# Performance work log

Measured on AMD Instinct MI355X. Metric: run time of the kernel, lower is better.

## Reference

```python
import jax, jax.numpy as jnp
import numpy as np

B, T, IN_DIM = 32, 512, 16
F_DIM, N_AGG, N_HEADS = 128, 32, 4


def _ln(x, g, b, eps=1e-5):
    m = jnp.mean(x, axis=-1, keepdims=True)
    v = jnp.var(x, axis=-1, keepdims=True)
    return (x - m) * jax.lax.rsqrt(v + eps) * g + b


def _masked_sab(X, mask, wq, bq, wk, bk, wv, bv, wo, bo, g0, be0, g1, be1):
    # Set-Transformer style SAB = MAB(X, X) with key-side masking.
    Bn, Tn, _ = X.shape
    Dh = F_DIM // N_HEADS
    Q = X @ wq + bq
    K = X @ wk + bk
    V = X @ wv + bv
    Qh = Q.reshape(Bn, Tn, N_HEADS, Dh)
    Kh = K.reshape(Bn, Tn, N_HEADS, Dh)
    Vh = V.reshape(Bn, Tn, N_HEADS, Dh)
    scores = jnp.einsum('bqhd,bkhd->bhqk', Qh, Kh) / np.float32(np.sqrt(Dh))
    scores = jnp.where(mask[:, None, None, :] > 0, scores, jnp.float32(-1e9))
    A = jax.nn.softmax(scores, axis=-1)
    O = Q + jnp.einsum('bhqk,bkhd->bqhd', A, Vh).reshape(Bn, Tn, F_DIM)
    O = _ln(O, g0, be0)
    O = O + jax.nn.relu(O @ wo + bo)
    return _ln(O, g1, be1)


def setup_inputs():
    key = jax.random.key(0)
    ks = list(jax.random.split(key, 16))

    def g(k, shape):
        return jax.random.uniform(k, shape, jnp.float32, -1.0, 1.0) / np.float32(np.sqrt(shape[0]))

    inp = {
        'X': jax.random.normal(ks[0], (B, T, IN_DIM), dtype=jnp.float32),
        'mask': jax.random.bernoulli(ks[1], 0.8, (B, T)).astype(jnp.float32),
    }
    i = 2
    for suf, din in (('0', IN_DIM), ('1', F_DIM)):
        kk = jax.random.split(ks[i], 4); i += 1
        inp['wq' + suf] = g(kk[0], (din, F_DIM)); inp['bq' + suf] = jnp.zeros((F_DIM,), jnp.float32)
        inp['wk' + suf] = g(kk[1], (din, F_DIM)); inp['bk' + suf] = jnp.zeros((F_DIM,), jnp.float32)
        inp['wv' + suf] = g(kk[2], (din, F_DIM)); inp['bv' + suf] = jnp.zeros((F_DIM,), jnp.float32)
        inp['wo' + suf] = g(kk[3], (F_DIM, F_DIM)); inp['bo' + suf] = jnp.zeros((F_DIM,), jnp.float32)
        inp['g0' + suf] = jnp.ones((F_DIM,), jnp.float32); inp['be0' + suf] = jnp.zeros((F_DIM,), jnp.float32)
        inp['g1' + suf] = jnp.ones((F_DIM,), jnp.float32); inp['be1' + suf] = jnp.zeros((F_DIM,), jnp.float32)
    inp['wti'] = g(ks[i], (F_DIM, F_DIM)); i += 1
    inp['bti'] = jnp.zeros((F_DIM,), jnp.float32)
    inp['was'] = g(ks[i], (F_DIM, N_AGG)); i += 1
    inp['bas'] = jnp.zeros((N_AGG,), jnp.float32)
    d_cat = 2 * F_DIM * N_AGG + IN_DIM + F_DIM
    inp['wto'] = g(ks[i], (d_cat, F_DIM)); i += 1
    inp['bto'] = jnp.zeros((F_DIM,), jnp.float32)
    inp['gto'] = jnp.ones((F_DIM,), jnp.float32)
    inp['btoln'] = jnp.zeros((F_DIM,), jnp.float32)
    return inp


def reference(X, mask, wq0, bq0, wk0, bk0, wv0, bv0, wo0, bo0, g00, be00, g10, be10,
              wq1, bq1, wk1, bk1, wv1, bv1, wo1, bo1, g01, be01, g11, be11,
              wti, bti, was, bas, wto, bto, gto, btoln):
    m = mask[..., None]                                  # [B,T,1]
    Xp = _masked_sab(X, mask, wq0, bq0, wk0, bk0, wv0, bv0, wo0, bo0, g00, be00, g10, be10) * m
    Xp = _masked_sab(Xp, mask, wq1, bq1, wk1, bk1, wv1, bv1, wo1, bo1, g01, be01, g11, be11) * m
    Xp = (Xp @ wti + bti) * m
    # masked softmax over tracks (dim 1); max is taken over ALL tracks as in original
    s = Xp @ was + bas                                   # [B,T,A]
    num = jnp.exp(s - jnp.max(s, axis=1, keepdims=True)) * m
    att = num / (jnp.sum(num, axis=1, keepdims=True) + 1e-16)
    edges = jnp.einsum('btf,bta->baft', Xp, att)         # [B,A,F,T] -- dominant buffer
    min_elem = jnp.min(edges, axis=-1) - 1.0             # [B,A,F]
    mk = mask[:, None, None, :]                          # [B,1,1,T]
    max_pooled = jnp.max(edges * mk + (1.0 - mk) * min_elem[..., None], axis=-1)
    n_tracks = jnp.sum(mask, axis=-1)[:, None, None]
    n_tracks = jnp.where(n_tracks == 0, jnp.float32(1.0), n_tracks)
    mean_pooled = jnp.sum(edges * mk, axis=-1) / n_tracks
    agg = jnp.concatenate([max_pooled, mean_pooled], axis=-1).reshape(X.shape[0], -1)  # [B, 2*F*A]
    agg_rep = jnp.broadcast_to(agg[:, None, :], (X.shape[0], X.shape[1], agg.shape[-1]))
    Hcat = jnp.concatenate([X, Xp, agg_rep], axis=-1)    # [B,T, 2*F*A + in + F]
    out = jax.nn.relu(_ln(Hcat @ wto + bto, gto, btoln)) * m
    return out, agg
```

## Files before the change

kernel.cpp:

```cpp
#include <hip/hip_runtime.h>
#include <hip/hip_bf16.h>

#define BB 32
#define TT 512
#define IND 16
#define FD 128
#define NAGG 32

typedef unsigned short ushortt;
typedef unsigned int uintt;
typedef __attribute__((ext_vector_type(8))) short bf16x8;
typedef __attribute__((ext_vector_type(4))) short s16x4;
typedef __attribute__((ext_vector_type(4))) float f32x4;

__device__ __forceinline__ short f2b(float x) {
  union { __hip_bfloat16 h; short s; } u;
  u.h = __float2bfloat16(x);
  return u.s;
}

#define MFMA_16x16x32(A, B, C) __builtin_amdgcn_mfma_f32_16x16x32_bf16(A, B, C, 0, 0, 0)

#define GEMM128(WT, c00, c01, c10, c11)                                        \
  {                                                                            \
    _Pragma("unroll") for (int ks = 0; ks < 4; ks++) {                         \
      bf16x8 a0 = *(const bf16x8*)&Xb[l15][ks * 32 + g * 8];                   \
      bf16x8 a1 = *(const bf16x8*)&Xb[16 + l15][ks * 32 + g * 8];              \
      bf16x8 b0 = *(const bf16x8*)((WT) + (size_t)c0 * 128 + ks * 32 + g * 8); \
      bf16x8 b1 = *(const bf16x8*)((WT) + (size_t)c1 * 128 + ks * 32 + g * 8); \
      c00 = MFMA_16x16x32(a0, b0, c00);                                        \
      c01 = MFMA_16x16x32(a0, b1, c01);                                        \
      c10 = MFMA_16x16x32(a1, b0, c10);                                        \
      c11 = MFMA_16x16x32(a1, b1, c11);                                        \
    }                                                                          \
  }

__global__ void prep_w_k(const float* __restrict__ wo0, const float* __restrict__ wq1,
                         const float* __restrict__ wk1, const float* __restrict__ wv1,
                         const float* __restrict__ wo1, const float* __restrict__ wti,
                         const float* __restrict__ wto, const float* __restrict__ was,
                         ushortt* __restrict__ Wt) {
  int m = blockIdx.x >> 2;
  int slab = blockIdx.x & 3;
  int tid = threadIdx.x;
  if (m == 7) {
    __shared__ float t[32][33];
    int iloc = tid >> 3, c4 = (tid & 7) * 4;
    *(float4*)&t[iloc][c4] = *(const float4*)(was + (size_t)(slab * 32 + iloc) * 32 + c4);
    __syncthreads();
    int a = tid & 31, ch = tid >> 5;
    short p[4];
#pragma unroll
    for (int k = 0; k < 4; k++) p[k] = f2b(t[ch * 4 + k][a]);
    *(s16x4*)(Wt + (size_t)7 * 16384 + (size_t)a * 128 + slab * 32 + ch * 4) = *(s16x4*)p;
  } else {
    const float* src = m == 0 ? wo0 : m == 1 ? wq1 : m == 2 ? wk1
                     : m == 3 ? wv1 : m == 4 ? wo1 : m == 5 ? wti : wto + IND * FD;
    __shared__ float t[32][132];
    int r = tid >> 3, c16 = (tid & 7) * 16;
    const float4* s4 = (const float4*)(src + (size_t)(slab * 32 + r) * 128 + c16);
#pragma unroll
    for (int jj = 0; jj < 4; jj++) *(float4*)&t[r][c16 + jj * 4] = s4[jj];
    __syncthreads();
    int f = tid >> 1, ih = (tid & 1) * 16;
    short p[16];
#pragma unroll
    for (int k = 0; k < 16; k++) p[k] = f2b(t[ih + k][f]);
    ushortt* dst = Wt + (size_t)m * 16384 + (size_t)f * 128 + slab * 32 + ih;
    *(bf16x8*)dst = *(bf16x8*)&p[0];
    *(bf16x8*)(dst + 8) = *(bf16x8*)&p[8];
  }
}

__global__ void proj16_k(const float* __restrict__ X,
                         const float* __restrict__ wq, const float* __restrict__ bq,
                         const float* __restrict__ wk, const float* __restrict__ bk,
                         const float* __restrict__ wv, const float* __restrict__ bv,
                         float* __restrict__ Q, ushortt* __restrict__ Kb,
                         ushortt* __restrict__ Vt) {
  int base = blockIdx.x * 8;
  int b = base >> 9;
  int tloc = base & 511;
  int f = threadIdx.x;
  __shared__ float xs[8][IND];
  {
    int rr = f >> 4, ii = f & 15;
    xs[rr][ii] = X[(size_t)(base + rr) * IND + ii];
  }
  __syncthreads();
  float qa[8], ka[8], va[8];
  float bqf = bq[f], bkf = bk[f], bvf = bv[f];
#pragma unroll
  for (int rr = 0; rr < 8; rr++) { qa[rr] = bqf; ka[rr] = bkf; va[rr] = bvf; }
#pragma unroll
  for (int i = 0; i < IND; i++) {
    float wqv = wq[i * FD + f], wkv = wk[i * FD + f], wvv = wv[i * FD + f];
#pragma unroll
    for (int rr = 0; rr < 8; rr++) {
      float x = xs[rr][i];
      qa[rr] += x * wqv; ka[rr] += x * wkv; va[rr] += x * wvv;
    }
  }
  short vp[8];
#pragma unroll
  for (int rr = 0; rr < 8; rr++) {
    size_t o = (size_t)(base + rr) * FD + f;
    Q[o] = qa[rr];
    Kb[o] = (ushortt)f2b(ka[rr]);
    vp[rr] = f2b(va[rr]);
  }
  *(bf16x8*)&Vt[((size_t)(b * FD) + f) * 512 + tloc] = *(bf16x8*)vp;
}

__global__ __launch_bounds__(256, 3) void attn_k(const float* __restrict__ Q,
                                                 const ushortt* __restrict__ Kb,
                                                 const ushortt* __restrict__ Vt,
                                                 const float* __restrict__ mask,
                                                 float* __restrict__ Ores) {
  int b = blockIdx.x >> 4;
  int qt = blockIdx.x & 15;
  int tid = threadIdx.x;
  int w = tid >> 6;
  int lane = tid & 63;
  int l15 = lane & 15, g = lane >> 4;

  __shared__ __align__(16) short qp_s[4 * 32 * 40];
  __shared__ __align__(16) short k_s[2][32 * 136];
  __shared__ __align__(16) short vt_s[2][128 * 40];
  __shared__ __align__(16) float msk_s[512];
  __shared__ __align__(16) float xch[4][32];

  const float scale = 0.17677669529663688f;

  msk_s[tid] = mask[b * TT + tid];
  msk_s[256 + tid] = mask[b * TT + 256 + tid];

  int sr = tid >> 3, sc8 = tid & 7;
  size_t qbase = ((size_t)(b * TT + qt * 32 + sr)) * FD + sc8 * 16;
  {
    const float4* src = (const float4*)(Q + qbase);
#pragma unroll
    for (int jj = 0; jj < 4; jj++) {
      float4 v4 = src[jj];
      *(s16x4*)&qp_s[sr * 136 + sc8 * 16 + jj * 4] =
          (s16x4){f2b(v4.x * scale), f2b(v4.y * scale), f2b(v4.z * scale),
                  f2b(v4.w * scale)};
    }
  }

  bf16x8 kr[2], vr[2];
  const ushortt* KbB = Kb + (size_t)b * TT * FD;
  const ushortt* VtB = Vt + (size_t)b * FD * 512;

#define LOAD_TILE(kt)                                                              \
  {                                                                                \
    const ushortt* kbp = KbB + (size_t)(kt) * 32 * FD;                             \
    _Pragma("unroll") for (int is = 0; is < 2; is++) {                             \
      int idx = tid + is * 256;                                                    \
      kr[is] = *(const bf16x8*)(kbp + (idx >> 4) * FD + (idx & 15) * 8);           \
      vr[is] = *(const bf16x8*)(VtB + (size_t)(idx >> 2) * 512 + (kt) * 32 +       \
                                (idx & 3) * 8);                                    \
    }                                                                              \
  }
#define WRITE_TILE(buf)                                                            \
  {                                                                                \
    _Pragma("unroll") for (int is = 0; is < 2; is++) {                             \
      int idx = tid + is * 256;                                                    \
      *(bf16x8*)&k_s[buf][(idx >> 4) * 136 + (idx & 15) * 8] = kr[is];             \
      *(bf16x8*)&vt_s[buf][(idx >> 2) * 40 + (idx & 3) * 8] = vr[is];              \
    }                                                                              \
  }

  LOAD_TILE(0);
  WRITE_TILE(0);

  f32x4 o00 = {0.f, 0.f, 0.f, 0.f}, o01 = o00, o10 = o00, o11 = o00;
  float m0 = -1e30f, m1 = -1e30f, l0 = 0.f, l1 = 0.f;

  bf16x8 aq0, aq1;
  int cur = 0;
  int pw = w * 1280;

  for (int kt = 0; kt < 16; kt++) {
    __syncthreads();
    if (kt == 0) {
      aq0 = *(const bf16x8*)&qp_s[l15 * 136 + w * 32 + g * 8];
      aq1 = *(const bf16x8*)&qp_s[(16 + l15) * 136 + w * 32 + g * 8];
      __syncthreads();
    }
    if (kt < 15) LOAD_TILE(kt + 1);

    bf16x8 bk0 = *(const bf16x8*)&k_s[cur][l15 * 136 + w * 32 + g * 8];
    bf16x8 bk1 = *(const bf16x8*)&k_s[cur][(16 + l15) * 136 + w * 32 + g * 8];
    f32x4 zero = {0.f, 0.f, 0.f, 0.f};
    f32x4 st00 = MFMA_16x16x32(bk0, aq0, zero);
    f32x4 st01 = MFMA_16x16x32(bk0, aq1, zero);
    f32x4 st10 = MFMA_16x16x32(bk1, aq0, zero);
    f32x4 st11 = MFMA_16x16x32(bk1, aq1, zero);

    float4 mk0 = *(const float4*)&msk_s[kt * 32 + 4 * g];
    float4 mk1 = *(const float4*)&msk_s[kt * 32 + 16 + 4 * g];
    float x0[8], x1[8];
#pragma unroll
    for (int r = 0; r < 4; r++) {
      x0[r] = mk0[r] > 0.f ? st00[r] : -1e9f;
      x0[4 + r] = mk1[r] > 0.f ? st10[r] : -1e9f;
      x1[r] = mk0[r] > 0.f ? st01[r] : -1e9f;
      x1[4 + r] = mk1[r] > 0.f ? st11[r] : -1e9f;
    }
    float lm0 = x0[0], lm1 = x1[0];
#pragma unroll
    for (int i = 1; i < 8; i++) { lm0 = fmaxf(lm0, x0[i]); lm1 = fmaxf(lm1, x1[i]); }
    lm0 = fmaxf(lm0, __shfl_xor(lm0, 16));
    lm0 = fmaxf(lm0, __shfl_xor(lm0, 32));
    lm1 = fmaxf(lm1, __shfl_xor(lm1, 16));
    lm1 = fmaxf(lm1, __shfl_xor(lm1, 32));
    bool need = (lm0 > m0 + 8.f) || (lm1 > m1 + 8.f);
    if (__any(need)) {
      float mn0 = fmaxf(m0, lm0), mn1 = fmaxf(m1, lm1);
      float scv0 = __expf(m0 - mn0), scv1 = __expf(m1 - mn1);
      m0 = mn0; m1 = mn1;
      l0 *= scv0; l1 *= scv1;
      if (lane < 16) { xch[w][l15] = scv0; xch[w][16 + l15] = scv1; }
      float4 sa = *(const float4*)&xch[w][4 * g];
      float4 sb = *(const float4*)&xch[w][16 + 4 * g];
#pragma unroll
      for (int r = 0; r < 4; r++) {
        o00[r] *= sa[r]; o01[r] *= sa[r];
        o10[r] *= sb[r]; o11[r] *= sb[r];
      }
    }
    float p0[8], p1[8];
    float rs0 = 0.f, rs1 = 0.f;
#pragma unroll
    for (int i = 0; i < 8; i++) {
      p0[i] = __expf(x0[i] - m0); rs0 += p0[i];
      p1[i] = __expf(x1[i] - m1); rs1 += p1[i];
    }
    rs0 += __shfl_xor(rs0, 16); rs0 += __shfl_xor(rs0, 32);
    rs1 += __shfl_xor(rs1, 16); rs1 += __shfl_xor(rs1, 32);
    l0 += rs0; l1 += rs1;
    {
      uintt a0 = ((uintt)(ushortt)f2b(p0[1]) << 16) | (ushortt)f2b(p0[0]);
      uintt a1 = ((uintt)(ushortt)f2b(p0[3]) << 16) | (ushortt)f2b(p0[2]);
      uintt a2 = ((uintt)(ushortt)f2b(p0[5]) << 16) | (ushortt)f2b(p0[4]);
      uintt a3 = ((uintt)(ushortt)f2b(p0[7]) << 16) | (ushortt)f2b(p0[6]);
      uintt b0 = ((uintt)(ushortt)f2b(p1[1]) << 16) | (ushortt)f2b(p1[0]);
      uintt b1 = ((uintt)(ushortt)f2b(p1[3]) << 16) | (ushortt)f2b(p1[2]);
      uintt b2 = ((uintt)(ushortt)f2b(p1[5]) << 16) | (ushortt)f2b(p1[4]);
      uintt b3 = ((uintt)(ushortt)f2b(p1[7]) << 16) | (ushortt)f2b(p1[6]);
      *(uint2*)&qp_s[pw + l15 * 40 + 4 * g] = make_uint2(a0, a1);
      *(uint2*)&qp_s[pw + l15 * 40 + 16 + 4 * g] = make_uint2(a2, a3);
      *(uint2*)&qp_s[pw + (16 + l15) * 40 + 4 * g] = make_uint2(b0, b1);
      *(uint2*)&qp_s[pw + (16 + l15) * 40 + 16 + 4 * g] = make_uint2(b2, b3);
    }
    bf16x8 ap0 = *(const bf16x8*)&qp_s[pw + l15 * 40 + g * 8];
    bf16x8 ap1 = *(const bf16x8*)&qp_s[pw + (16 + l15) * 40 + g * 8];
    bf16x8 bv0 = *(const bf16x8*)&vt_s[cur][(w * 32 + l15) * 40 + g * 8];
    bf16x8 bv1 = *(const bf16x8*)&vt_s[cur][(w * 32 + 16 + l15) * 40 + g * 8];
    o00 = MFMA_16x16x32(ap0, bv0, o00);
    o01 = MFMA_16x16x32(ap0, bv1, o01);
    o10 = MFMA_16x16x32(ap1, bv0, o10);
    o11 = MFMA_16x16x32(ap1, bv1, o11);

    if (kt < 15) WRITE_TILE(cur ^ 1);
    cur ^= 1;
  }
  if (lane < 16) { xch[w][l15] = l0; xch[w][16 + l15] = l1; }
  float4 la = *(const float4*)&xch[w][4 * g];
  float4 lb = *(const float4*)&xch[w][16 + 4 * g];
  size_t rowbase = (size_t)(b * TT + qt * 32);
#pragma unroll
  for (int r = 0; r < 4; r++) {
    int q0r = 4 * g + r;
    size_t base0 = (rowbase + q0r) * FD + w * 32 + l15;
    Ores[base0] = Q[base0] + o00[r] / la[r];
    Ores[base0 + 16] = Q[base0 + 16] + o01[r] / la[r];
    int q1r = 16 + 4 * g + r;
    size_t base1 = (rowbase + q1r) * FD + w * 32 + l15;
    Ores[base1] = Q[base1] + o10[r] / lb[r];
    Ores[base1 + 16] = Q[base1 + 16] + o11[r] / lb[r];
  }
#undef LOAD_TILE
#undef WRITE_TILE
}

__device__ __forceinline__ void ln32(float (*A)[132], short (*Xb)[136], int lane, int w,
                                     const float* __restrict__ gg,
                                     const float* __restrict__ bb,
                                     const float* mk, bool applyMask) {
  float ga = gg[lane], gb = gg[lane + 64], ba = bb[lane], b2 = bb[lane + 64];
  for (int j = 0; j < 8; j++) {
    int rr = w * 8 + j;
    float a = A[rr][lane], c = A[rr][lane + 64];
    float s = a + c, ss = a * a + c * c;
#pragma unroll
    for (int o = 32; o > 0; o >>= 1) { s += __shfl_xor(s, o); ss += __shfl_xor(ss, o); }
    float mean = s * (1.f / 128.f);
    float var = ss * (1.f / 128.f) - mean * mean;
    float rs = rsqrtf(var + 1e-5f);
    float m = applyMask ? mk[rr] : 1.f;
    float y0 = ((a - mean) * rs * ga + ba) * m;
    float y1 = ((c - mean) * rs * gb + b2) * m;
    A[rr][lane] = y0; A[rr][lane + 64] = y1;
    Xb[rr][lane] = f2b(y0); Xb[rr][lane + 64] = f2b(y1);
  }
}

__global__ __launch_bounds__(256) void post_proj_k(
    const float* __restrict__ Ores, const float* __restrict__ mask,
    const ushortt* __restrict__ wot, const float* __restrict__ bo,
    const float* __restrict__ g0, const float* __restrict__ be0,
    const float* __restrict__ g1, const float* __restrict__ be1,
    const ushortt* __restrict__ wqt, const float* __restrict__ bq,
    const ushortt* __restrict__ wkt, const float* __restrict__ bk,
    const ushortt* __restrict__ wvt, const float* __restrict__ bv,
    float* __restrict__ Q, ushortt* __restrict__ Kb, ushortt* __restrict__ Vt) {
  int base = blockIdx.x * 32;
  int b = base >> 9;
  int tloc = base & 511;
  int tid = threadIdx.x;
  int w = tid >> 6, lane = tid & 63;
  int l15 = lane & 15, g = lane >> 4;

  __shared__ float A32[32][132];
  __shared__ __align__(16) short Xb[32][136];
  __shared__ float mk[32];

  {
    int r = tid >> 3, c = (tid & 7) * 16;
    const float4* src = (const float4*)(Ores + (size_t)(base + r) * FD + c);
#pragma unroll
    for (int jj = 0; jj < 4; jj++) *(float4*)&A32[r][c + jj * 4] = src[jj];
  }
  if (tid < 32) mk[tid] = mask[base + tid];
  __syncthreads();
  ln32(A32, Xb, lane, w, g0, be0, mk, false);
  __syncthreads();

  int c0 = w * 32 + l15, c1 = c0 + 16;
  f32x4 f00 = {0.f, 0.f, 0.f, 0.f}, f01 = f00, f10 = f00, f11 = f00;
  GEMM128(wot, f00, f01, f10, f11);
  float bo0 = bo[c0], bo1 = bo[c1];
#pragma unroll
  for (int r = 0; r < 4; r++) {
    int r0 = g * 4 + r, r1 = 16 + r0;
    A32[r0][c0] += fmaxf(f00[r] + bo0, 0.f);
    A32[r0][c1] += fmaxf(f01[r] + bo1, 0.f);
    A32[r1][c0] += fmaxf(f10[r] + bo0, 0.f);
    A32[r1][c1] += fmaxf(f11[r] + bo1, 0.f);
  }
  __syncthreads();
  ln32(A32, Xb, lane, w, g1, be1, mk, true);
  __syncthreads();

  {
    f32x4 q00 = {0.f, 0.f, 0.f, 0.f}, q01 = q00, q10 = q00, q11 = q00;
    GEMM128(wqt, q00, q01, q10, q11);
    float bq0 = bq[c0], bq1 = bq[c1];
#pragma unroll
    for (int r = 0; r < 4; r++) {
      int r0 = g * 4 + r, r1 = 16 + r0;
      Q[(size_t)(base + r0) * FD + c0] = q00[r] + bq0;
      Q[(size_t)(base + r0) * FD + c1] = q01[r] + bq1;
      Q[(size_t)(base + r1) * FD + c0] = q10[r] + bq0;
      Q[(size_t)(base + r1) * FD + c1] = q11[r] + bq1;
    }
  }
  {
    f32x4 k00 = {0.f, 0.f, 0.f, 0.f}, k01 = k00, k10 = k00, k11 = k00;
    GEMM128(wkt, k00, k01, k10, k11);
    float bk0 = bk[c0], bk1 = bk[c1];
#pragma unroll
    for (int r = 0; r < 4; r++) {
      int r0 = g * 4 + r, r1 = 16 + r0;
      Kb[(size_t)(base + r0) * FD + c0] = (ushortt)f2b(k00[r] + bk0);
      Kb[(size_t)(base + r0) * FD + c1] = (ushortt)f2b(k01[r] + bk1);
      Kb[(size_t)(base + r1) * FD + c0] = (ushortt)f2b(k10[r] + bk0);
      Kb[(size_t)(base + r1) * FD + c1] = (ushortt)f2b(k11[r] + bk1);
    }
  }
  {
    f32x4 v00 = {0.f, 0.f, 0.f, 0.f}, v01 = v00, v10 = v00, v11 = v00;
    GEMM128(wvt, v00, v01, v10, v11);
    float bv0 = bv[c0], bv1 = bv[c1];
    short p[4];
#pragma unroll
    for (int k = 0; k < 4; k++) p[k] = f2b(v00[k] + bv0);
    *(s16x4*)&Vt[((size_t)b * FD + c0) * 512 + tloc + g * 4] = *(s16x4*)p;
#pragma unroll
    for (int k = 0; k < 4; k++) p[k] = f2b(v01[k] + bv1);
    *(s16x4*)&Vt[((size_t)b * FD + c1) * 512 + tloc + g * 4] = *(s16x4*)p;
#pragma unroll
    for (int k = 0; k < 4; k++) p[k] = f2b(v10[k] + bv0);
    *(s16x4*)&Vt[((size_t)b * FD + c0) * 512 + tloc + 16 + g * 4] = *(s16x4*)p;
#pragma unroll
    for (int k = 0; k < 4; k++) p[k] = f2b(v11[k] + bv1);
    *(s16x4*)&Vt[((size_t)b * FD + c1) * 512 + tloc + 16 + g * 4] = *(s16x4*)p;
  }
}

__global__ __launch_bounds__(256) void post_ti_k(
    const float* __restrict__ Ores, const float* __restrict__ mask,
    const ushortt* __restrict__ wot, const float* __restrict__ bo,
    const float* __restrict__ g0, const float* __restrict__ be0,
    const float* __restrict__ g1, const float* __restrict__ be1,
    const ushortt* __restrict__ wtit, const float* __restrict__ bti,
    const ushortt* __restrict__ wast, const float* __restrict__ bas,
    float* __restrict__ Xp2, float* __restrict__ S) {
  int base = blockIdx.x * 32;
  int tid = threadIdx.x;
  int w = tid >> 6, lane = tid & 63;
  int l15 = lane & 15, g = lane >> 4;

  __shared__ float A32[32][132];
  __shared__ __align__(16) short Xb[32][136];
  __shared__ float mk[32];

  {
    int r = tid >> 3, c = (tid & 7) * 16;
    const float4* src = (const float4*)(Ores + (size_t)(base + r) * FD + c);
#pragma unroll
    for (int jj = 0; jj < 4; jj++) *(float4*)&A32[r][c + jj * 4] = src[jj];
  }
  if (tid < 32) mk[tid] = mask[base + tid];
  __syncthreads();
  ln32(A32, Xb, lane, w, g0, be0, mk, false);
  __syncthreads();

  int c0 = w * 32 + l15, c1 = c0 + 16;
  f32x4 f00 = {0.f, 0.f, 0.f, 0.f}, f01 = f00, f10 = f00, f11 = f00;
  GEMM128(wot, f00, f01, f10, f11);
  float bo0 = bo[c0], bo1 = bo[c1];
#pragma unroll
  for (int r = 0; r < 4; r++) {
    int r0 = g * 4 + r, r1 = 16 + r0;
    A32[r0][c0] += fmaxf(f00[r] + bo0, 0.f);
    A32[r0][c1] += fmaxf(f01[r] + bo1, 0.f);
    A32[r1][c0] += fmaxf(f10[r] + bo0, 0.f);
    A32[r1][c1] += fmaxf(f11[r] + bo1, 0.f);
  }
  __syncthreads();
  ln32(A32, Xb, lane, w, g1, be1, mk, true);
  __syncthreads();

  f32x4 t00 = {0.f, 0.f, 0.f, 0.f}, t01 = t00, t10 = t00, t11 = t00;
  GEMM128(wtit, t00, t01, t10, t11);
  float bti0 = bti[c0], bti1 = bti[c1];
  short pk[16];
#pragma unroll
  for (int r = 0; r < 4; r++) {
    int r0 = g * 4 + r, r1 = 16 + r0;
    float v00 = (t00[r] + bti0) * mk[r0];
    float v01 = (t01[r] + bti1) * mk[r0];
    float v10 = (t10[r] + bti0) * mk[r1];
    float v11 = (t11[r] + bti1) * mk[r1];
    Xp2[(size_t)(base + r0) * FD + c0] = v00;
    Xp2[(size_t)(base + r0) * FD + c1] = v01;
    Xp2[(size_t)(base + r1) * FD + c0] = v10;
    Xp2[(size_t)(base + r1) * FD + c1] = v11;
    pk[r * 4 + 0] = f2b(v00);
    pk[r * 4 + 1] = f2b(v01);
    pk[r * 4 + 2] = f2b(v10);
    pk[r * 4 + 3] = f2b(v11);
  }
  __syncthreads();
#pragma unroll
  for (int r = 0; r < 4; r++) {
    int r0 = g * 4 + r, r1 = 16 + r0;
    Xb[r0][c0] = pk[r * 4 + 0];
    Xb[r0][c1] = pk[r * 4 + 1];
    Xb[r1][c0] = pk[r * 4 + 2];
    Xb[r1][c1] = pk[r * 4 + 3];
  }
  __syncthreads();
  if (w < 2) {
    int a0 = w * 16 + l15;
    f32x4 s0 = {0.f, 0.f, 0.f, 0.f}, s1 = s0;
#pragma unroll
    for (int ks = 0; ks < 4; ks++) {
      bf16x8 aa0 = *(const bf16x8*)&Xb[l15][ks * 32 + g * 8];
      bf16x8 aa1 = *(const bf16x8*)&Xb[16 + l15][ks * 32 + g * 8];
      bf16x8 bb0 = *(const bf16x8*)(wast + (size_t)a0 * 128 + ks * 32 + g * 8);
      s0 = MFMA_16x16x32(aa0, bb0, s0);
      s1 = MFMA_16x16x32(aa1, bb0, s1);
    }
    float bas0 = bas[a0];
#pragma unroll
    for (int r = 0; r < 4; r++) {
      int r0 = g * 4 + r;
      S[(size_t)(base + r0) * NAGG + a0] = s0[r] + bas0;
      S[(size_t)(base + 16 + r0) * NAGG + a0] = s1[r] + bas0;
    }
  }
}

__global__ void soft_t(const float* __restrict__ S, const float* __restrict__ mask,
                       float* __restrict__ att) {
  int b = blockIdx.x >> 5, a = blockIdx.x & 31;
  int tid = threadIdx.x;
  __shared__ float red[2];
  float sv[4], mv[4];
#pragma unroll
  for (int j = 0; j < 4; j++) {
    int t = tid + j * 128;
    sv[j] = S[(size_t)(b * TT + t) * NAGG + a];
    mv[j] = mask[b * TT + t];
  }
  float mx = fmaxf(fmaxf(sv[0], sv[1]), fmaxf(sv[2], sv[3]));
#pragma unroll
  for (int o = 32; o > 0; o >>= 1) mx = fmaxf(mx, __shfl_xor(mx, o));
  if ((tid & 63) == 0) red[tid >> 6] = mx;
  __syncthreads();
  mx = fmaxf(red[0], red[1]);
  __syncthreads();
  float e[4];
  float sm = 0.f;
#pragma unroll
  for (int j = 0; j < 4; j++) {
    e[j] = __expf(sv[j] - mx) * mv[j];
    sm += e[j];
  }
#pragma unroll
  for (int o = 32; o > 0; o >>= 1) sm += __shfl_xor(sm, o);
  if ((tid & 63) == 0) red[tid >> 6] = sm;
  __syncthreads();
  float inv = 1.f / (red[0] + red[1] + 1e-16f);
  float* dst = att + ((size_t)(b * NAGG + a)) * TT;
#pragma unroll
  for (int j = 0; j < 4; j++) dst[tid + j * 128] = e[j] * inv;
}

__global__ __launch_bounds__(256) void pool_k2(const float* __restrict__ Xp2,
                                               const float* __restrict__ att,
                                               const float* __restrict__ mask,
                                               float* __restrict__ pmax,
                                               float* __restrict__ pmin,
                                               float* __restrict__ psum) {
  int bid = blockIdx.x;
  int b = bid >> 4;
  int tc = (bid >> 2) & 3;
  int fg = (bid >> 1) & 1;
  int ag = bid & 1;
  int tid = threadIdx.x;
  __shared__ float xp_s[128][68];
  __shared__ float att_s[16][128];
  __shared__ float ms[128];
  {
    int r = tid >> 1, half = tid & 1;
    const float4* src =
        (const float4*)(Xp2 + ((size_t)(b * TT + tc * 128 + r)) * FD + fg * 64 + half * 32);
#pragma unroll
    for (int j = 0; j < 8; j++) *(float4*)&xp_s[r][half * 32 + j * 4] = src[j];
  }
  {
    int a = tid >> 4, t8 = (tid & 15) * 8;
    const float4* src =
        (const float4*)(att + ((size_t)(b * NAGG + ag * 16 + a)) * TT + tc * 128 + t8);
    *(float4*)&att_s[a][t8] = src[0];
    *(float4*)&att_s[a][t8 + 4] = src[1];
  }
  if (tid < 128) ms[tid] = mask[b * TT + tc * 128 + tid];
  __syncthreads();
  int fl = tid & 63, h = tid >> 6;
  float mn[4], mx[4], sm[4];
#pragma unroll
  for (int a = 0; a < 4; a++) { mn[a] = 1e30f; mx[a] = -1e30f; sm[a] = 0.f; }
#pragma unroll 4
  for (int t = 0; t < 128; t++) {
    float e0 = xp_s[t][fl];
    bool keep = ms[t] > 0.f;
#pragma unroll
    for (int a = 0; a < 4; a++) {
      float e = e0 * att_s[h * 4 + a][t];
      mn[a] = fminf(mn[a], e);
      mx[a] = keep ? fmaxf(mx[a], e) : mx[a];
      sm[a] = keep ? sm[a] + e : sm[a];
    }
  }
#pragma unroll
  for (int a = 0; a < 4; a++) {
    int aa = ag * 16 + h * 4 + a;
    size_t idx = ((size_t)((b * 4 + tc) * 32 + aa)) * 128 + fg * 64 + fl;
    pmax[idx] = mx[a];
    pmin[idx] = mn[a];
    psum[idx] = sm[a];
  }
}

__global__ void combine_k(const float* __restrict__ pmax, const float* __restrict__ pmin,
                          const float* __restrict__ psum, const float* __restrict__ mask,
                          float* __restrict__ aggF, float* __restrict__ agg_out) {
  int b = blockIdx.x >> 5, a = blockIdx.x & 31;
  int f = threadIdx.x;
  __shared__ float red[2];
  float ntp = 0.f;
#pragma unroll
  for (int j = 0; j < 4; j++) ntp += (mask[b * TT + f + j * 128] > 0.f) ? 1.f : 0.f;
#pragma unroll
  for (int o = 32; o > 0; o >>= 1) ntp += __shfl_xor(ntp, o);
  if ((f & 63) == 0) red[f >> 6] = ntp;
  __syncthreads();
  float nt = red[0] + red[1];
  float mx = -1e30f, mn = 1e30f, sm = 0.f;
#pragma unroll
  for (int tc = 0; tc < 4; tc++) {
    size_t idx = ((size_t)((b * 4 + tc) * 32 + a)) * 128 + f;
    mx = fmaxf(mx, pmax[idx]);
    mn = fminf(mn, pmin[idx]);
    sm += psum[idx];
  }
  bool anyUn = nt < 511.5f;
  float mp = anyUn ? fmaxf(mx, mn - 1.f) : mx;
  float mean = sm / (nt == 0.f ? 1.f : nt);
  size_t bs = (size_t)b * 8192 + (size_t)a * 256;
  aggF[bs + f] = mp;
  aggF[bs + 128 + f] = mean;
  agg_out[bs + f] = mp;
  agg_out[bs + 128 + f] = mean;
}

__global__ void aggmm_k(const float* __restrict__ aggF, const float* __restrict__ wto,
                        float* __restrict__ part) {
  int b = blockIdx.x >> 5, cc = blockIdx.x & 31;
  int f = threadIdx.x;
  __shared__ float ag[256];
  ag[f] = aggF[(size_t)b * 8192 + cc * 256 + f];
  ag[128 + f] = aggF[(size_t)b * 8192 + cc * 256 + 128 + f];
  __syncthreads();
  const float* w = wto + ((size_t)(IND + FD) + cc * 256) * FD;
  float a0 = 0.f, a1 = 0.f, a2 = 0.f, a3 = 0.f;
#pragma unroll 4
  for (int j = 0; j < 256; j += 4) {
    a0 += ag[j] * w[(size_t)j * FD + f];
    a1 += ag[j + 1] * w[(size_t)(j + 1) * FD + f];
    a2 += ag[j + 2] * w[(size_t)(j + 2) * FD + f];
    a3 += ag[j + 3] * w[(size_t)(j + 3) * FD + f];
  }
  part[(size_t)(b * 32 + cc) * FD + f] = (a0 + a1) + (a2 + a3);
}

__global__ __launch_bounds__(256) void final_k(
    const float* __restrict__ X, const float* __restrict__ Xp2,
    const float* __restrict__ part, const ushortt* __restrict__ wtot,
    const float* __restrict__ wto, const float* __restrict__ bto,
    const float* __restrict__ gto, const float* __restrict__ btoln,
    const float* __restrict__ mask, float* __restrict__ out) {
  int base = blockIdx.x * 32;
  int b = base >> 9;
  int tid = threadIdx.x;
  int w = tid >> 6, lane = tid & 63;
  int l15 = lane & 15, g = lane >> 4;
  __shared__ float A32[32][132];
  __shared__ __align__(16) short Xb[32][136];
  __shared__ float xss[32][17];
  __shared__ float psum_s[128];
  __shared__ float mk[32];
  {
    int r = tid >> 3, c = (tid & 7) * 16;
    const float4* src = (const float4*)(Xp2 + (size_t)(base + r) * FD + c);
#pragma unroll
    for (int jj = 0; jj < 4; jj++) {
      float4 v = src[jj];
      *(s16x4*)&Xb[r][c + jj * 4] = (s16x4){f2b(v.x), f2b(v.y), f2b(v.z), f2b(v.w)};
    }
  }
  {
    int r = tid >> 3, ii = (tid & 7) * 2;
    xss[r][ii] = X[(size_t)(base + r) * IND + ii];
    xss[r][ii + 1] = X[(size_t)(base + r) * IND + ii + 1];
  }
  if (tid < 32) mk[tid] = mask[base + tid];
  if (tid < 128) {
    float ps = 0.f;
#pragma unroll 8
    for (int cc = 0; cc < 32; cc++) ps += part[(size_t)(b * 32 + cc) * FD + tid];
    psum_s[tid] = ps;
  }
  __syncthreads();
  int c0 = w * 32 + l15, c1 = c0 + 16;
  f32x4 q00 = {0.f, 0.f, 0.f, 0.f}, q01 = q00, q10 = q00, q11 = q00;
  GEMM128(wtot, q00, q01, q10, q11);
  float wx0[16], wx1[16];
#pragma unroll
  for (int i = 0; i < 16; i++) { wx0[i] = wto[i * FD + c0]; wx1[i] = wto[i * FD + c1]; }
  float add0 = bto[c0] + psum_s[c0], add1 = bto[c1] + psum_s[c1];
#pragma unroll
  for (int r = 0; r < 4; r++) {
    int r0 = g * 4 + r, r1 = 16 + r0;
    float x00 = q00[r] + add0, x01 = q01[r] + add1;
    float x10 = q10[r] + add0, x11 = q11[r] + add1;
#pragma unroll
    for (int i = 0; i < 16; i++) {
      x00 += xss[r0][i] * wx0[i];
      x01 += xss[r0][i] * wx1[i];
      x10 += xss[r1][i] * wx0[i];
      x11 += xss[r1][i] * wx1[i];
    }
    A32[r0][c0] = x00; A32[r0][c1] = x01;
    A32[r1][c0] = x10; A32[r1][c1] = x11;
  }
  __syncthreads();
  float ga = gto[lane], gb = gto[lane + 64], ba = btoln[lane], bb2 = btoln[lane + 64];
  for (int j = 0; j < 8; j++) {
    int rr = w * 8 + j;
    float a = A32[rr][lane], c = A32[rr][lane + 64];
    float s = a + c, ss = a * a + c * c;
#pragma unroll
    for (int o = 32; o > 0; o >>= 1) { s += __shfl_xor(s, o); ss += __shfl_xor(ss, o); }
    float mean = s * (1.f / 128.f);
    float var = ss * (1.f / 128.f) - mean * mean;
    float rs = rsqrtf(var + 1e-5f);
    float m = mk[rr];
    out[(size_t)(base + rr) * FD + lane] = fmaxf((a - mean) * rs * ga + ba, 0.f) * m;
    out[(size_t)(base + rr) * FD + lane + 64] = fmaxf((c - mean) * rs * gb + bb2, 0.f) * m;
  }
}

extern "C" void kernel_launch(void* const* d_in, const int* in_sizes, int n_in,
                              void* d_out, int out_size, void* d_ws, size_t ws_size,
                              hipStream_t stream) {
  const float* X    = (const float*)d_in[0];
  const float* mask = (const float*)d_in[1];
  const float* wq0 = (const float*)d_in[2];  const float* bq0 = (const float*)d_in[3];
  const float* wk0 = (const float*)d_in[4];  const float* bk0 = (const float*)d_in[5];
  const float* wv0 = (const float*)d_in[6];  const float* bv0 = (const float*)d_in[7];
  const float* wo0 = (const float*)d_in[8];  const float* bo0 = (const float*)d_in[9];
  const float* g00 = (const float*)d_in[10]; const float* be00 = (const float*)d_in[11];
  const float* g10 = (const float*)d_in[12]; const float* be10 = (const float*)d_in[13];
  const float* wq1 = (const float*)d_in[14]; const float* bq1 = (const float*)d_in[15];
  const float* wk1 = (const float*)d_in[16]; const float* bk1 = (const float*)d_in[17];
  const float* wv1 = (const float*)d_in[18]; const float* bv1 = (const float*)d_in[19];
  const float* wo1 = (const float*)d_in[20]; const float* bo1 = (const float*)d_in[21];
  const float* g01 = (const float*)d_in[22]; const float* be01 = (const float*)d_in[23];
  const float* g11 = (const float*)d_in[24]; const float* be11 = (const float*)d_in[25];
  const float* wti = (const float*)d_in[26]; const float* bti = (const float*)d_in[27];
  const float* was = (const float*)d_in[28]; const float* bas = (const float*)d_in[29];
  const float* wto = (const float*)d_in[30]; const float* bto = (const float*)d_in[31];
  const float* gto = (const float*)d_in[32]; const float* btoln = (const float*)d_in[33];

  const size_t BIG = (size_t)BB * TT * FD;
  float* ws = (float*)d_ws;
  float* Qf = ws;
  ushortt* Kb = (ushortt*)(ws + BIG);
  ushortt* Vt = (ushortt*)(ws + BIG + BIG / 2);
  float* Ores = Qf;
  float* Xp2 = ws + BIG;
  float* S    = ws + 2 * BIG;
  float* att  = ws + 2 * BIG + 524288;
  float* aggF = ws + 2 * BIG + 1048576;
  float* part = ws + 2 * BIG + 1310720;
  ushortt* Wt = (ushortt*)(ws + 2 * BIG + 1441792);
  float* pmax = ws;
  float* pmin = ws + 524288;
  float* psum = ws + 1048576;

  ushortt* wo0t = Wt;
  ushortt* wq1t = Wt + 16384;
  ushortt* wk1t = Wt + 2 * 16384;
  ushortt* wv1t = Wt + 3 * 16384;
  ushortt* wo1t = Wt + 4 * 16384;
  ushortt* wtit = Wt + 5 * 16384;
  ushortt* wtot = Wt + 6 * 16384;
  ushortt* wast = Wt + 7 * 16384;

  float* out_main = (float*)d_out;
  float* out_agg  = (float*)d_out + BIG;

  int nrb = BB * TT / 8;
  int nrb32 = BB * TT / 32;
  prep_w_k<<<32, 256, 0, stream>>>(wo0, wq1, wk1, wv1, wo1, wti, wto, was, Wt);
  proj16_k<<<nrb, 128, 0, stream>>>(X, wq0, bq0, wk0, bk0, wv0, bv0, Qf, Kb, Vt);
  attn_k<<<BB * 16, 256, 0, stream>>>(Qf, Kb, Vt, mask, Ores);
  post_proj_k<<<nrb32, 256, 0, stream>>>(Ores, mask, wo0t, bo0, g00, be00, g10, be10,
                                         wq1t, bq1, wk1t, bk1, wv1t, bv1, Qf, Kb, Vt);
  attn_k<<<BB * 16, 256, 0, stream>>>(Qf, Kb, Vt, mask, Ores);
  post_ti_k<<<nrb32, 256, 0, stream>>>(Ores, mask, wo1t, bo1, g01, be01, g11, be11,
                                       wtit, bti, wast, bas, Xp2, S);
  soft_t<<<BB * NAGG, 128, 0, stream>>>(S, mask, att);
  pool_k2<<<BB * 16, 256, 0, stream>>>(Xp2, att, mask, pmax, pmin, psum);
  combine_k<<<BB * NAGG, 128, 0, stream>>>(pmax, pmin, psum, mask, aggF, out_agg);
  aggmm_k<<<BB * 32, 128, 0, stream>>>(aggF, wto, part);
  final_k<<<nrb32, 256, 0, stream>>>(X, Xp2, part, wtot, wto, bto, gto, btoln, mask, out_main);
}
```

Baseline: 145.1 us.

## Split attention over key halves with separate combine kernel

```diff
diff --git a/kernel.cpp b/kernel.cpp
--- a/kernel.cpp
+++ b/kernel.cpp
@@ -17,6 +17,11 @@
   union { __hip_bfloat16 h; short s; } u;
   u.h = __float2bfloat16(x);
   return u.s;
+}
+__device__ __forceinline__ float b2fu(ushortt x) {
+  union { float f; uintt u; } v;
+  v.u = ((uintt)x) << 16;
+  return v.f;
 }
 
 #define MFMA_16x16x32(A, B, C) __builtin_amdgcn_mfma_f32_16x16x32_bf16(A, B, C, 0, 0, 0)
@@ -116,9 +121,13 @@
                                                  const ushortt* __restrict__ Kb,
                                                  const ushortt* __restrict__ Vt,
                                                  const float* __restrict__ mask,
-                                                 float* __restrict__ Ores) {
-  int b = blockIdx.x >> 4;
-  int qt = blockIdx.x & 15;
+                                                 ushortt* __restrict__ Opart,
+                                                 float* __restrict__ Mbuf,
+                                                 float* __restrict__ Lbuf) {
+  int bid = blockIdx.x;
+  int ks = bid & 1;
+  int qt = (bid >> 1) & 15;
+  int b = bid >> 5;
   int tid = threadIdx.x;
   int w = tid >> 6;
   int lane = tid & 63;
@@ -171,7 +180,8 @@
     }                                                                              \
   }
 
-  LOAD_TILE(0);
+  int ktbase = ks * 8;
+  LOAD_TILE(ktbase);
   WRITE_TILE(0);
 
   f32x4 o00 = {0.f, 0.f, 0.f, 0.f}, o01 = o00, o10 = o00, o11 = o00;
@@ -181,14 +191,15 @@
   int cur = 0;
   int pw = w * 1280;
 
-  for (int kt = 0; kt < 16; kt++) {
+  for (int kt8 = 0; kt8 < 8; kt8++) {
+    int kt = ktbase + kt8;
     __syncthreads();
-    if (kt == 0) {
+    if (kt8 == 0) {
       aq0 = *(const bf16x8*)&qp_s[l15 * 136 + w * 32 + g * 8];
       aq1 = *(const bf16x8*)&qp_s[(16 + l15) * 136 + w * 32 + g * 8];
       __syncthreads();
     }
-    if (kt < 15) LOAD_TILE(kt + 1);
+    if (kt8 < 7) LOAD_TILE(kt + 1);
 
     bf16x8 bk0 = *(const bf16x8*)&k_s[cur][l15 * 136 + w * 32 + g * 8];
     bf16x8 bk1 = *(const bf16x8*)&k_s[cur][(16 + l15) * 136 + w * 32 + g * 8];
@@ -263,26 +274,58 @@
     o10 = MFMA_16x16x32(ap1, bv0, o10);
     o11 = MFMA_16x16x32(ap1, bv1, o11);
 
-    if (kt < 15) WRITE_TILE(cur ^ 1);
+    if (kt8 < 7) WRITE_TILE(cur ^ 1);
     cur ^= 1;
   }
-  if (lane < 16) { xch[w][l15] = l0; xch[w][16 + l15] = l1; }
-  float4 la = *(const float4*)&xch[w][4 * g];
-  float4 lb = *(const float4*)&xch[w][16 + 4 * g];
-  size_t rowbase = (size_t)(b * TT + qt * 32);
+  ushortt* op = Opart + ((size_t)ks * BB + b) * TT * FD;
 #pragma unroll
   for (int r = 0; r < 4; r++) {
     int q0r = 4 * g + r;
-    size_t base0 = (rowbase + q0r) * FD + w * 32 + l15;
-    Ores[base0] = Q[base0] + o00[r] / la[r];
-    Ores[base0 + 16] = Q[base0 + 16] + o01[r] / la[r];
+    size_t o0 = (size_t)(qt * 32 + q0r) * FD + w * 32 + l15;
+    op[o0] = (ushortt)f2b(o00[r]);
+    op[o0 + 16] = (ushortt)f2b(o01[r]);
     int q1r = 16 + 4 * g + r;
-    size_t base1 = (rowbase + q1r) * FD + w * 32 + l15;
-    Ores[base1] = Q[base1] + o10[r] / lb[r];
-    Ores[base1 + 16] = Q[base1 + 16] + o11[r] / lb[r];
+    size_t o1 = (size_t)(qt * 32 + q1r) * FD + w * 32 + l15;
+    op[o1] = (ushortt)f2b(o10[r]);
+    op[o1 + 16] = (ushortt)f2b(o11[r]);
+  }
+  if (lane < 16) {
+    size_t t0 = (size_t)(b * TT + qt * 32) + l15;
+    size_t t1 = t0 + 16;
+    Mbuf[(t0 * 4 + w) * 2 + ks] = m0;
+    Mbuf[(t1 * 4 + w) * 2 + ks] = m1;
+    Lbuf[(t0 * 4 + w) * 2 + ks] = l0;
+    Lbuf[(t1 * 4 + w) * 2 + ks] = l1;
   }
 #undef LOAD_TILE
 #undef WRITE_TILE
+}
+
+__global__ void attn_comb_k(const float* __restrict__ Q, const ushortt* __restrict__ Opart,
+                            const float* __restrict__ Mbuf, const float* __restrict__ Lbuf,
+                            float* __restrict__ Ores) {
+  int bq = blockIdx.x;
+  int b = bq >> 4, qt = bq & 15;
+  int tid = threadIdx.x;
+  int f = tid & 127, rg = tid >> 7;
+  int h = f >> 5;
+  const ushortt* op0 = Opart + (size_t)b * TT * FD;
+  const ushortt* op1 = Opart + ((size_t)BB + b) * TT * FD;
+#pragma unroll 4
+  for (int r2 = 0; r2 < 16; r2++) {
+    int row = rg * 16 + r2;
+    size_t t = (size_t)(b * TT + qt * 32 + row);
+    size_t ml = (t * 4 + h) * 2;
+    float m0 = Mbuf[ml], m1 = Mbuf[ml + 1];
+    float l0 = Lbuf[ml], l1 = Lbuf[ml + 1];
+    float m = fmaxf(m0, m1);
+    float w0 = __expf(m0 - m), w1 = __expf(m1 - m);
+    float l = l0 * w0 + l1 * w1;
+    size_t idx = (size_t)(qt * 32 + row) * FD + f;
+    float o0 = b2fu(op0[idx]), o1 = b2fu(op1[idx]);
+    size_t gidx = t * FD + f;
+    Ores[gidx] = Q[gidx] + (o0 * w0 + o1 * w1) / l;
+  }
 }
 
 __device__ __forceinline__ void ln32(float (*A)[132], short (*Xb)[136], int lane, int w,
@@ -751,6 +794,10 @@
   float* aggF = ws + 2 * BIG + 1048576;
   float* part = ws + 2 * BIG + 1310720;
   ushortt* Wt = (ushortt*)(ws + 2 * BIG + 1441792);
+  float* spbase = ws + 2 * BIG + 1441792 + 65536;
+  ushortt* Opart = (ushortt*)spbase;
+  float* Mbuf = spbase + BIG;
+  float* Lbuf = spbase + BIG + 131072;
   float* pmax = ws;
   float* pmin = ws + 524288;
   float* psum = ws + 1048576;
@@ -771,10 +818,12 @@
   int nrb32 = BB * TT / 32;
   prep_w_k<<<32, 256, 0, stream>>>(wo0, wq1, wk1, wv1, wo1, wti, wto, was, Wt);
   proj16_k<<<nrb, 128, 0, stream>>>(X, wq0, bq0, wk0, bk0, wv0, bv0, Qf, Kb, Vt);
-  attn_k<<<BB * 16, 256, 0, stream>>>(Qf, Kb, Vt, mask, Ores);
+  attn_k<<<BB * 32, 256, 0, stream>>>(Qf, Kb, Vt, mask, Opart, Mbuf, Lbuf);
+  attn_comb_k<<<BB * 16, 256, 0, stream>>>(Qf, Opart, Mbuf, Lbuf, Ores);
   post_proj_k<<<nrb32, 256, 0, stream>>>(Ores, mask, wo0t, bo0, g00, be00, g10, be10,
                                          wq1t, bq1, wk1t, bk1, wv1t, bv1, Qf, Kb, Vt);
-  attn_k<<<BB * 16, 256, 0, stream>>>(Qf, Kb, Vt, mask, Ores);
+  attn_k<<<BB * 32, 256, 0, stream>>>(Qf, Kb, Vt, mask, Opart, Mbuf, Lbuf);
+  attn_comb_k<<<BB * 16, 256, 0, stream>>>(Qf, Opart, Mbuf, Lbuf, Ores);
   post_ti_k<<<nrb32, 256, 0, stream>>>(Ores, mask, wo1t, bo1, g01, be01, g11, be11,
                                        wtit, bti, wast, bas, Xp2, S);
   soft_t<<<BB * NAGG, 128, 0, stream>>>(S, mask, att);
```

Result: slower. 155.1 us (+6.9%).
